# Kernel tuning notes

Hardware: AMD Instinct MI355X
Metric: run time of the kernel (lower is better)

## Reference

```python
import jax, jax.numpy as jnp
import numpy as np

DIM = 512; HEADS = 8; B = 8; H = 64; W = 64; SPLIT = 8
H_SP, W_SP = H, SPLIT          # idx = 0: vertical stripes (full height, split_size wide)
S = H_SP * W_SP                # tokens per window
HEAD_DIM = DIM // HEADS


def _win(x, heads):
    # [B, C, H, W] -> [B*nW, heads, S, C//heads]
    b, c, h, w = x.shape
    d = c // heads
    x = x.reshape(b, heads, d, h // H_SP, H_SP, w // W_SP, W_SP)
    x = x.transpose(0, 3, 5, 1, 4, 6, 2)  # b, nh, nw, heads, H_sp, W_sp, d
    return x.reshape(b * (h // H_SP) * (w // W_SP), heads, S, d)


def _unwin(x, b, c):
    # [B*nW, heads, S, d] -> [B, H*W, C]
    heads, d = x.shape[1], x.shape[-1]
    nh, nw = H // H_SP, W // W_SP
    x = x.reshape(b, nh, nw, heads, H_SP, W_SP, d)
    x = x.transpose(0, 1, 4, 2, 5, 3, 6)  # b, nh, H_sp, nw, W_sp, heads, d
    return x.reshape(b, H * W, c)


def _dwconv(x, w, bias):
    # depthwise 3x3, padding 1 (the get_v lepe conv)
    y = jax.lax.conv_general_dilated(
        x, w, window_strides=(1, 1), padding='SAME',
        feature_group_count=x.shape[1],
        dimension_numbers=('NCHW', 'OIHW', 'NCHW'))
    return y + bias[None, :, None, None]


def setup_inputs() -> dict:
    key = jax.random.key(0)
    k1, k2, k3 = jax.random.split(key, 3)
    temp = jax.random.normal(k1, (3, B, DIM, H, W), dtype=jnp.float32)
    polar_coord = jax.random.uniform(k2, (B, H, W, 2), dtype=jnp.float32)
    conv_w = jax.random.normal(k3, (DIM, 1, 3, 3), dtype=jnp.float32) * 0.02
    conv_b = jnp.zeros((DIM,), dtype=jnp.float32)
    return {'temp': temp, 'polar_coord': polar_coord, 'conv_w': conv_w, 'conv_b': conv_b}


def reference(temp, polar_coord, conv_w, conv_b):
    q, k, v = temp[0], temp[1], temp[2]            # each [B, C, H, W]
    scale = HEAD_DIM ** -0.5

    # lepe: depthwise conv on v, added AFTER attn @ v (second positional bias)
    lepe = _win(_dwconv(v, conv_w, conv_b), HEADS)  # [BnW, heads, S, d]

    qw = _win(q, HEADS) * scale
    kw = _win(k, HEADS)
    vw = _win(v, HEADS)

    # polar RPE (idx=0 branch): relative phi within each window, added BEFORE softmax-replacement
    phi = polar_coord[..., 1][:, None]              # [B, 1, H, W]
    phiw = _win(phi, 1)[..., 0]                     # [BnW, 1, S]
    rpe = phiw[..., :, None] - phiw[..., None, :]   # [BnW, 1, S, S], broadcast over heads

    score = jnp.einsum('bhid,bhjd->bhij', qw, kw) + rpe
    # L1-normalize along keys, then cosine score activation (idx=0 branch)
    l1 = jnp.sum(jnp.abs(score), axis=-1, keepdims=True)
    attn = 1.0 - jnp.cos(score / (l1 + 1e-8) * (jnp.pi / 2))

    out = jnp.einsum('bhij,bhjd->bhid', attn, vw) + lepe
    return _unwin(out, B, DIM)                      # [B, H*W, C]
```

## Files before the change

kernel.cpp:

```cpp
#include <hip/hip_runtime.h>
#include <cstdint>
#include <cstddef>


typedef float f32x4 __attribute__((ext_vector_type(4)));
typedef __bf16 bf16x8 __attribute__((ext_vector_type(8)));

__device__ __forceinline__ unsigned short f2bf(float f) {
  union { float f; unsigned int u; } t; t.f = f;
  unsigned int u = t.u;
  return (unsigned short)((u + 0x7fffu + ((u >> 16) & 1u)) >> 16);
}

__global__ __launch_bounds__(256, 2)
void lepe_kernel(const float* __restrict__ temp,
                 const float* __restrict__ cw,
                 const float* __restrict__ cbias,
                 float* __restrict__ out)
{
  __shared__ float tile[64 * 256];
  const int t  = threadIdx.x;
  const int x  = t & 63;
  const int w0 = t >> 6;
  const int bz = blockIdx.x;
  const int b  = bz >> 7;
  const int cg = (bz >> 4) & 7;
  const int y0 = (bz & 15) * 4;
  const int cb = cg * 64;
  const float* vimg = temp + (size_t)16 * 2097152 + (size_t)b * 2097152;

  #pragma unroll 2
  for (int i = 0; i < 16; ++i) {
    const int cl = i * 4 + w0;
    const int c  = __builtin_amdgcn_readfirstlane(cb + cl);
    const float* wp = cw + c * 9;
    float wgt[9];
    #pragma unroll
    for (int j = 0; j < 9; ++j) wgt[j] = wp[j];
    const float bias = cbias[c];
    const float* vc = vimg + (size_t)c * 4096;

    float m[6], l[6], r[6];
    #pragma unroll
    for (int j = 0; j < 6; ++j) {
      const int yy = y0 - 1 + j;
      float v = 0.f;
      if (yy >= 0 && yy <= 63) v = vc[yy * 64 + x];
      m[j] = v;
      const float lu = __shfl_up(v, 1);
      const float rd = __shfl_down(v, 1);
      l[j] = (x == 0)  ? 0.f : lu;
      r[j] = (x == 63) ? 0.f : rd;
    }
    #pragma unroll
    for (int oy = 0; oy < 4; ++oy) {
      float a = bias;
      #pragma unroll
      for (int ky = 0; ky < 3; ++ky) {
        const int j = oy + ky;
        a += l[j] * wgt[ky * 3 + 0] + m[j] * wgt[ky * 3 + 1] + r[j] * wgt[ky * 3 + 2];
      }
      const int p = oy * 64 + x;
      tile[cl * 256 + (p ^ (cl & 31))] = a;
    }
  }
  __syncthreads();

  const int c0 = (t & 15) * 4;
  const int ps = t >> 4;
  #pragma unroll 4
  for (int i = 0; i < 16; ++i) {
    const int p = ps + i * 16;
    const int y = p >> 6, xx = p & 63;
    float4 o;
    o.x = tile[(c0 + 0) * 256 + (p ^ ((c0 + 0) & 31))];
    o.y = tile[(c0 + 1) * 256 + (p ^ ((c0 + 1) & 31))];
    o.z = tile[(c0 + 2) * 256 + (p ^ ((c0 + 2) & 31))];
    o.w = tile[(c0 + 3) * 256 + (p ^ ((c0 + 3) & 31))];
    *(float4*)&out[((size_t)b * 4096 + (y0 + y) * 64 + xx) * 512 + cb + c0] = o;
  }
}

__global__ __launch_bounds__(256, 2)
void attn_kernel(const float* __restrict__ temp,
                 const float* __restrict__ polar,
                 float* __restrict__ out)
{
  __shared__ __align__(16) unsigned short sm_kv[9216];
  __shared__ __align__(16) unsigned short sm_q[64 * 72];
  __shared__ __align__(16) unsigned short sm_attn[4 * 16 * 40];
  __shared__ float sm_phi[512];

  const int t    = threadIdx.x;
  const int lane = t & 63;
  const int wv   = t >> 6;
  const int l15  = lane & 15;
  const int q4   = lane >> 4;

  const int bid0 = blockIdx.x;
  const int bid  = ((bid0 & 7) << 9) | (bid0 >> 3);
  const int wi  = bid >> 6;
  const int hh  = (bid >> 3) & 7;
  const int rt  = bid & 7;
  const int b   = wi >> 3;
  const int wx  = wi & 7;

  const size_t img = (size_t)512 * 4096;
  const size_t base_bh = (size_t)b * img + (size_t)(hh * 64) * 4096 + wx * 8;
  const float* qp = temp + base_bh;
  const float* kp = temp + 8 * img + base_bh;
  const float* vp = temp + 16 * img + base_bh;

  for (int i = t; i < 512; i += 256) {
    const int y = i >> 3, xl = i & 7;
    sm_phi[i] = polar[((size_t)b * 4096 + y * 64 + wx * 8 + xl) * 2 + 1];
  }

  #pragma unroll
  for (int it = 0; it < 4; ++it) {
    const int idx = it * 256 + t;
    const int h   = idx & 1;
    const int dch = (idx >> 1) & 63;
    const int y8  = idx >> 7;
    const float4 v4 = *(const float4*)(qp + (size_t)dch * 4096 + (rt * 8 + y8) * 64 + h * 4);
    const int tok = y8 * 8 + h * 4;
    sm_q[(tok + 0) * 72 + dch] = f2bf(v4.x);
    sm_q[(tok + 1) * 72 + dch] = f2bf(v4.y);
    sm_q[(tok + 2) * 72 + dch] = f2bf(v4.z);
    sm_q[(tok + 3) * 72 + dch] = f2bf(v4.w);
  }
  __syncthreads();

  bf16x8 qf[2];
  #pragma unroll
  for (int kc = 0; kc < 2; ++kc)
    qf[kc] = __builtin_bit_cast(
        bf16x8, *(const uint4*)&sm_q[(wv * 16 + l15) * 72 + kc * 32 + q4 * 8]);

  f32x4 acc[32];
  #pragma unroll
  for (int jt = 0; jt < 32; ++jt) acc[jt] = (f32x4){0.f, 0.f, 0.f, 0.f};

  unsigned short* smk = sm_kv;
  #pragma unroll
  for (int ch = 0; ch < 4; ++ch) {
    __syncthreads();
    #pragma unroll
    for (int it = 0; it < 8; ++it) {
      const int idx = it * 256 + t;
      const int h   = idx & 1;
      const int dch = (idx >> 1) & 63;
      const int yl  = idx >> 7;
      const float4 v4 = *(const float4*)(kp + (size_t)dch * 4096 + (ch * 16 + yl) * 64 + h * 4);
      const int tok = yl * 8 + h * 4;
      smk[(tok + 0) * 72 + dch] = f2bf(v4.x);
      smk[(tok + 1) * 72 + dch] = f2bf(v4.y);
      smk[(tok + 2) * 72 + dch] = f2bf(v4.z);
      smk[(tok + 3) * 72 + dch] = f2bf(v4.w);
    }
    __syncthreads();
    #pragma unroll
    for (int j8 = 0; j8 < 8; ++j8) {
      const int jt = ch * 8 + j8;
      const bf16x8 kf0 = __builtin_bit_cast(
          bf16x8, *(const uint4*)&smk[(j8 * 16 + l15) * 72 + q4 * 8]);
      const bf16x8 kf1 = __builtin_bit_cast(
          bf16x8, *(const uint4*)&smk[(j8 * 16 + l15) * 72 + 32 + q4 * 8]);
      acc[jt] = __builtin_amdgcn_mfma_f32_16x16x32_bf16(qf[0], kf0, acc[jt], 0, 0, 0);
      acc[jt] = __builtin_amdgcn_mfma_f32_16x16x32_bf16(qf[1], kf1, acc[jt], 0, 0, 0);
    }
  }

  float phi_r[4];
  #pragma unroll
  for (int r = 0; r < 4; ++r)
    phi_r[r] = sm_phi[rt * 64 + wv * 16 + q4 * 4 + r];
  float l1p[4] = {0.f, 0.f, 0.f, 0.f};
  #pragma unroll
  for (int jt = 0; jt < 32; ++jt) {
    const float phi_c = sm_phi[jt * 16 + l15];
    #pragma unroll
    for (int r = 0; r < 4; ++r) {
      const float s = acc[jt][r] * 0.125f + (phi_r[r] - phi_c);
      acc[jt][r] = s;
      l1p[r] += fabsf(s);
    }
  }
  #pragma unroll
  for (int r = 0; r < 4; ++r) {
    float v = l1p[r];
    v += __shfl_xor(v, 1, 16);
    v += __shfl_xor(v, 2, 16);
    v += __shfl_xor(v, 4, 16);
    v += __shfl_xor(v, 8, 16);
    l1p[r] = 1.5707963267948966f / (v + 1e-8f);
  }

  f32x4 oacc[4];
  #pragma unroll
  for (int nt = 0; nt < 4; ++nt) oacc[nt] = (f32x4){0.f, 0.f, 0.f, 0.f};

  unsigned short* smv = sm_kv;
  unsigned short* sma = sm_attn + wv * (16 * 40);
  #pragma unroll
  for (int vc = 0; vc < 4; ++vc) {
    __syncthreads();
    #pragma unroll
    for (int it = 0; it < 8; ++it) {
      const int idx = it * 256 + t;
      const int h   = idx & 1;
      const int dch = (idx >> 1) & 63;
      const int yl  = idx >> 7;
      const float4 v4 = *(const float4*)(vp + (size_t)dch * 4096 + (vc * 16 + yl) * 64 + h * 4);
      uint2 p;
      p.x = (unsigned)f2bf(v4.x) | ((unsigned)f2bf(v4.y) << 16);
      p.y = (unsigned)f2bf(v4.z) | ((unsigned)f2bf(v4.w) << 16);
      *(uint2*)&smv[dch * 136 + yl * 8 + h * 4] = p;
    }
    __syncthreads();
    #pragma unroll
    for (int k2 = 0; k2 < 4; ++k2) {
      const int jt0 = vc * 8 + k2 * 2;
      #pragma unroll
      for (int jl = 0; jl < 2; ++jl) {
        const int jt = jt0 + jl;
        #pragma unroll
        for (int r = 0; r < 4; ++r) {
          const float x  = acc[jt][r] * l1p[r];
          const float sn = __sinf(0.5f * x);
          sma[(q4 * 4 + r) * 40 + jl * 16 + l15] = f2bf(2.f * sn * sn);
        }
      }
      const bf16x8 af = __builtin_bit_cast(
          bf16x8, *(const uint4*)&sma[l15 * 40 + q4 * 8]);
      #pragma unroll
      for (int nt = 0; nt < 4; ++nt) {
        const bf16x8 vf = __builtin_bit_cast(
            bf16x8, *(const uint4*)&smv[(nt * 16 + l15) * 136 + k2 * 32 + q4 * 8]);
        oacc[nt] = __builtin_amdgcn_mfma_f32_16x16x32_bf16(af, vf, oacc[nt], 0, 0, 0);
      }
    }
  }

  #pragma unroll
  for (int r = 0; r < 4; ++r) {
    const int srow = rt * 64 + wv * 16 + q4 * 4 + r;
    const int y = srow >> 3, xl = srow & 7;
    const size_t obase = ((size_t)b * 4096 + y * 64 + wx * 8 + xl) * 512 + hh * 64;
    #pragma unroll
    for (int nt = 0; nt < 4; ++nt) {
      const size_t oi = obase + nt * 16 + l15;
      out[oi] += oacc[nt][r];
    }
  }
}

extern "C" void kernel_launch(void* const* d_in, const int* in_sizes, int n_in,
                              void* d_out, int out_size, void* d_ws, size_t ws_size,
                              hipStream_t stream) {
  const float* temp  = (const float*)d_in[0];
  const float* polar = (const float*)d_in[1];
  const float* cw    = (const float*)d_in[2];
  const float* cb    = (const float*)d_in[3];
  float* out = (float*)d_out;

  lepe_kernel<<<1024, 256, 0, stream>>>(temp, cw, cb, out);
  attn_kernel<<<4096, 256, 0, stream>>>(temp, polar, out);
}
```

Baseline: 516.6 us.

## Prefetch next K/V chunk into registers while computing current chunk in attention

The K and V staging loops now issue global loads for the next 16-row chunk into a register buffer before the MFMA work on the current chunk, then convert and write them to shared memory after a barrier. The first V chunk is loaded before the L1 normalization step so its latency is hidden behind that math. V conversion uses the packed v_cvt_pk_bf16_f32 instruction instead of manual rounding. This is meant to hide global memory latency behind compute, at the cost of 32 extra float registers per thread, which may pressure the 2-blocks-per-SM occupancy target alongside the 128-register accumulator array.

Result: faster. 492.7 us (-4.6%).

```diff
diff --git a/kernel.cpp b/kernel.cpp
--- a/kernel.cpp
+++ b/kernel.cpp
@@ -10,6 +10,12 @@
   union { float f; unsigned int u; } t; t.f = f;
   unsigned int u = t.u;
   return (unsigned short)((u + 0x7fffu + ((u >> 16) & 1u)) >> 16);
+}
+
+__device__ __forceinline__ unsigned cvtpk(float lo, float hi) {
+  unsigned r;
+  asm("v_cvt_pk_bf16_f32 %0, %1, %2" : "=v"(r) : "v"(lo), "v"(hi));
+  return r;
 }
 
 __global__ __launch_bounds__(256, 2)
@@ -111,23 +117,42 @@
   const float* kp = temp + 8 * img + base_bh;
   const float* vp = temp + 16 * img + base_bh;
 
+  const int s_h   = t & 1;
+  const int s_dch = (t >> 1) & 63;
+  const int s_y   = t >> 7;
+
   for (int i = t; i < 512; i += 256) {
     const int y = i >> 3, xl = i & 7;
     sm_phi[i] = polar[((size_t)b * 4096 + y * 64 + wx * 8 + xl) * 2 + 1];
   }
 
+  float4 ld[8];
+  #pragma unroll
+  for (int it = 0; it < 8; ++it) {
+    const int yl = it * 2 + s_y;
+    ld[it] = *(const float4*)(kp + (size_t)s_dch * 4096 + yl * 64 + s_h * 4);
+  }
+
   #pragma unroll
   for (int it = 0; it < 4; ++it) {
-    const int idx = it * 256 + t;
-    const int h   = idx & 1;
-    const int dch = (idx >> 1) & 63;
-    const int y8  = idx >> 7;
-    const float4 v4 = *(const float4*)(qp + (size_t)dch * 4096 + (rt * 8 + y8) * 64 + h * 4);
-    const int tok = y8 * 8 + h * 4;
-    sm_q[(tok + 0) * 72 + dch] = f2bf(v4.x);
-    sm_q[(tok + 1) * 72 + dch] = f2bf(v4.y);
-    sm_q[(tok + 2) * 72 + dch] = f2bf(v4.z);
-    sm_q[(tok + 3) * 72 + dch] = f2bf(v4.w);
+    const int y8 = it * 2 + s_y;
+    const float4 v4 = *(const float4*)(qp + (size_t)s_dch * 4096 + (rt * 8 + y8) * 64 + s_h * 4);
+    const int tok = y8 * 8 + s_h * 4;
+    sm_q[(tok + 0) * 72 + s_dch] = f2bf(v4.x);
+    sm_q[(tok + 1) * 72 + s_dch] = f2bf(v4.y);
+    sm_q[(tok + 2) * 72 + s_dch] = f2bf(v4.z);
+    sm_q[(tok + 3) * 72 + s_dch] = f2bf(v4.w);
+  }
+
+  unsigned short* smk = sm_kv;
+  #pragma unroll
+  for (int it = 0; it < 8; ++it) {
+    const int yl  = it * 2 + s_y;
+    const int tok = yl * 8 + s_h * 4;
+    smk[(tok + 0) * 72 + s_dch] = f2bf(ld[it].x);
+    smk[(tok + 1) * 72 + s_dch] = f2bf(ld[it].y);
+    smk[(tok + 2) * 72 + s_dch] = f2bf(ld[it].z);
+    smk[(tok + 3) * 72 + s_dch] = f2bf(ld[it].w);
   }
   __syncthreads();
 
@@ -141,24 +166,15 @@
   #pragma unroll
   for (int jt = 0; jt < 32; ++jt) acc[jt] = (f32x4){0.f, 0.f, 0.f, 0.f};
 
-  unsigned short* smk = sm_kv;
   #pragma unroll
   for (int ch = 0; ch < 4; ++ch) {
-    __syncthreads();
-    #pragma unroll
-    for (int it = 0; it < 8; ++it) {
-      const int idx = it * 256 + t;
-      const int h   = idx & 1;
-      const int dch = (idx >> 1) & 63;
-      const int yl  = idx >> 7;
-      const float4 v4 = *(const float4*)(kp + (size_t)dch * 4096 + (ch * 16 + yl) * 64 + h * 4);
-      const int tok = yl * 8 + h * 4;
-      smk[(tok + 0) * 72 + dch] = f2bf(v4.x);
-      smk[(tok + 1) * 72 + dch] = f2bf(v4.y);
-      smk[(tok + 2) * 72 + dch] = f2bf(v4.z);
-      smk[(tok + 3) * 72 + dch] = f2bf(v4.w);
-    }
-    __syncthreads();
+    if (ch < 3) {
+      #pragma unroll
+      for (int it = 0; it < 8; ++it) {
+        const int yl = it * 2 + s_y;
+        ld[it] = *(const float4*)(kp + (size_t)s_dch * 4096 + ((ch + 1) * 16 + yl) * 64 + s_h * 4);
+      }
+    }
     #pragma unroll
     for (int j8 = 0; j8 < 8; ++j8) {
       const int jt = ch * 8 + j8;
@@ -169,6 +185,25 @@
       acc[jt] = __builtin_amdgcn_mfma_f32_16x16x32_bf16(qf[0], kf0, acc[jt], 0, 0, 0);
       acc[jt] = __builtin_amdgcn_mfma_f32_16x16x32_bf16(qf[1], kf1, acc[jt], 0, 0, 0);
     }
+    __syncthreads();
+    if (ch < 3) {
+      #pragma unroll
+      for (int it = 0; it < 8; ++it) {
+        const int yl  = it * 2 + s_y;
+        const int tok = yl * 8 + s_h * 4;
+        smk[(tok + 0) * 72 + s_dch] = f2bf(ld[it].x);
+        smk[(tok + 1) * 72 + s_dch] = f2bf(ld[it].y);
+        smk[(tok + 2) * 72 + s_dch] = f2bf(ld[it].z);
+        smk[(tok + 3) * 72 + s_dch] = f2bf(ld[it].w);
+      }
+      __syncthreads();
+    }
+  }
+
+  #pragma unroll
+  for (int it = 0; it < 8; ++it) {
+    const int yl = it * 2 + s_y;
+    ld[it] = *(const float4*)(vp + (size_t)s_dch * 4096 + yl * 64 + s_h * 4);
   }
 
   float phi_r[4];
@@ -196,28 +231,31 @@
     l1p[r] = 1.5707963267948966f / (v + 1e-8f);
   }
 
+  unsigned short* smv = sm_kv;
+  #pragma unroll
+  for (int it = 0; it < 8; ++it) {
+    const int yl = it * 2 + s_y;
+    uint2 p;
+    p.x = cvtpk(ld[it].x, ld[it].y);
+    p.y = cvtpk(ld[it].z, ld[it].w);
+    *(uint2*)&smv[s_dch * 136 + yl * 8 + s_h * 4] = p;
+  }
+  __syncthreads();
+
   f32x4 oacc[4];
   #pragma unroll
   for (int nt = 0; nt < 4; ++nt) oacc[nt] = (f32x4){0.f, 0.f, 0.f, 0.f};
 
-  unsigned short* smv = sm_kv;
   unsigned short* sma = sm_attn + wv * (16 * 40);
   #pragma unroll
   for (int vc = 0; vc < 4; ++vc) {
-    __syncthreads();
-    #pragma unroll
-    for (int it = 0; it < 8; ++it) {
-      const int idx = it * 256 + t;
-      const int h   = idx & 1;
-      const int dch = (idx >> 1) & 63;
-      const int yl  = idx >> 7;
-      const float4 v4 = *(const float4*)(vp + (size_t)dch * 4096 + (vc * 16 + yl) * 64 + h * 4);
-      uint2 p;
-      p.x = (unsigned)f2bf(v4.x) | ((unsigned)f2bf(v4.y) << 16);
-      p.y = (unsigned)f2bf(v4.z) | ((unsigned)f2bf(v4.w) << 16);
-      *(uint2*)&smv[dch * 136 + yl * 8 + h * 4] = p;
-    }
-    __syncthreads();
+    if (vc < 3) {
+      #pragma unroll
+      for (int it = 0; it < 8; ++it) {
+        const int yl = it * 2 + s_y;
+        ld[it] = *(const float4*)(vp + (size_t)s_dch * 4096 + ((vc + 1) * 16 + yl) * 64 + s_h * 4);
+      }
+    }
     #pragma unroll
     for (int k2 = 0; k2 < 4; ++k2) {
       const int jt0 = vc * 8 + k2 * 2;
@@ -240,6 +278,18 @@
         oacc[nt] = __builtin_amdgcn_mfma_f32_16x16x32_bf16(af, vf, oacc[nt], 0, 0, 0);
       }
     }
+    __syncthreads();
+    if (vc < 3) {
+      #pragma unroll
+      for (int it = 0; it < 8; ++it) {
+        const int yl = it * 2 + s_y;
+        uint2 p;
+        p.x = cvtpk(ld[it].x, ld[it].y);
+        p.y = cvtpk(ld[it].z, ld[it].w);
+        *(uint2*)&smv[s_dch * 136 + yl * 8 + s_h * 4] = p;
+      }
+      __syncthreads();
+    }
   }
 
   #pragma unroll
```
